# Performance work log

Measured on AMD Instinct MI355X. Metric: run time of the kernel, lower is better.

Reference implementation:

```python
import jax, jax.numpy as jnp
import numpy as np

N = 100000      # total nodes (batched graphs)
E = 1200000     # total edges
A = 256         # annotation size (hidden_size_orig)
H = 64          # gnn_h_size
T = 4           # num_edge_types
STEPS = 6       # num_timesteps
B = 64          # number of graphs in the batch
NUM_CLS = 2


def setup_inputs() -> dict:
    key = jax.random.key(0)
    ks = jax.random.split(key, 16)
    annotation = jax.random.normal(ks[0], (N, A), dtype=jnp.float32)
    src = jax.random.randint(ks[1], (E,), 0, N, dtype=jnp.int32)
    dst = jax.random.randint(ks[2], (E,), 0, N, dtype=jnp.int32)
    etypes = jax.random.randint(ks[3], (E,), 0, T, dtype=jnp.int32)
    graph_ids = jnp.sort(jax.random.randint(ks[4], (N,), 0, B, dtype=jnp.int32))

    def lin(k, fan_in, shape):
        return jax.random.normal(k, shape, dtype=jnp.float32) / np.sqrt(fan_in).astype(np.float32)

    params = {
        'reduce_W': lin(ks[5], A, (A, H)),
        'reduce_b': jnp.zeros((H,), jnp.float32),
        'edge_W': lin(ks[6], H, (T, H, H)),      # per-edge-type linear
        'edge_b': jnp.zeros((T, H), jnp.float32),
        'gru_Wi': lin(ks[7], H, (3 * H, H)),     # torch GRUCell layout: r,z,n
        'gru_bi': jnp.zeros((3 * H,), jnp.float32),
        'gru_Wh': lin(ks[8], H, (3 * H, H)),
        'gru_bh': jnp.zeros((3 * H,), jnp.float32),
        'gate_W': lin(ks[9], 2 * H, (2 * H, 1)),
        'gate_b': jnp.zeros((1,), jnp.float32),
        'out_W': lin(ks[10], 2 * H, (2 * H, NUM_CLS)),
        'out_b': jnp.zeros((NUM_CLS,), jnp.float32),
    }
    return dict(annotation=annotation, src=src, dst=dst, etypes=etypes,
                graph_ids=graph_ids, **params)


def reference(annotation, src, dst, etypes, graph_ids,
              reduce_W, reduce_b, edge_W, edge_b,
              gru_Wi, gru_bi, gru_Wh, gru_bh,
              gate_W, gate_b, out_W, out_b):
    # reduce_layer
    h0 = annotation @ reduce_W + reduce_b            # [N, H]

    def step(h, _):
        # per-edge-type linear on all nodes: [T, N, H]
        transformed = jnp.einsum('nh,thk->tnk', h, edge_W) + edge_b[:, None, :]
        msg = transformed[etypes, src]               # [E, H] gather per edge
        a = jax.ops.segment_sum(msg, dst, num_segments=N)  # scatter-add
        # GRUCell(a, h)
        gi = a @ gru_Wi.T + gru_bi
        gh = h @ gru_Wh.T + gru_bh
        i_r, i_z, i_n = jnp.split(gi, 3, axis=-1)
        h_r, h_z, h_n = jnp.split(gh, 3, axis=-1)
        r = jax.nn.sigmoid(i_r + h_r)
        z = jax.nn.sigmoid(i_z + h_z)
        n = jnp.tanh(i_n + r * h_n)
        h_new = (1.0 - z) * n + z * h
        return h_new, None

    h, _ = jax.lax.scan(step, h0, None, length=STEPS)

    feat = jnp.concatenate([h, h0], axis=-1)         # [N, 2H]

    # GlobalAttentionPooling: segment softmax over gate scores, weighted sum
    gate = feat @ gate_W + gate_b                    # [N, 1]
    gmax = jax.ops.segment_max(gate, graph_ids, num_segments=B)
    gmax = jnp.where(jnp.isfinite(gmax), gmax, 0.0)  # guard empty graphs
    e = jnp.exp(gate - gmax[graph_ids])
    denom = jax.ops.segment_sum(e, graph_ids, num_segments=B)
    alpha = e / denom[graph_ids]                     # [N, 1]
    readout = jax.ops.segment_sum(alpha * feat, graph_ids, num_segments=B)  # [B, 2H]

    logits = readout @ out_W + out_b                 # [B, 2]
    return logits
```

## Files before the change

kernel.cpp:

```cpp
#include <hip/hip_runtime.h>
#include <cstdint>
#include <cstddef>

#define N_NODES 100000
#define N_EDGES 1200000
#define ASIZE 256
#define HSIZE 64
#define NTYPES 4
#define NSTEPS 6
#define NGRAPH 64
#define PS 16

static __device__ __forceinline__ float sigmoidf_(float x) { return 1.0f / (1.0f + expf(-x)); }

__global__ void k_count(const int* __restrict__ dst, int* __restrict__ deg) {
    int e = blockIdx.x * 256 + threadIdx.x;
    if (e < N_EDGES) atomicAdd(&deg[dst[e]], 1);
}

__global__ void k_scan1(const int* __restrict__ deg, int* __restrict__ rs, int* __restrict__ part) {
    __shared__ int sh[256];
    int t = threadIdx.x;
    int base = blockIdx.x * 1024 + t * 4;
    int v0 = (base + 0 < N_NODES) ? deg[base + 0] : 0;
    int v1 = (base + 1 < N_NODES) ? deg[base + 1] : 0;
    int v2 = (base + 2 < N_NODES) ? deg[base + 2] : 0;
    int v3 = (base + 3 < N_NODES) ? deg[base + 3] : 0;
    int s = v0 + v1 + v2 + v3;
    sh[t] = s;
    __syncthreads();
    for (int off = 1; off < 256; off <<= 1) {
        int x = (t >= off) ? sh[t - off] : 0;
        __syncthreads();
        sh[t] += x;
        __syncthreads();
    }
    int excl = sh[t] - s;
    if (t == 255) part[blockIdx.x] = sh[255];
    if (base + 0 < N_NODES) rs[base + 0] = excl;
    if (base + 1 < N_NODES) rs[base + 1] = excl + v0;
    if (base + 2 < N_NODES) rs[base + 2] = excl + v0 + v1;
    if (base + 3 < N_NODES) rs[base + 3] = excl + v0 + v1 + v2;
}

__global__ void k_scan2(int* __restrict__ part, int* __restrict__ rs, int nb) {
    if (threadIdx.x == 0 && blockIdx.x == 0) {
        int run = 0;
        for (int i = 0; i < nb; ++i) { int v = part[i]; part[i] = run; run += v; }
        rs[N_NODES] = run;
    }
}

__global__ void k_scan3(int* __restrict__ rs, const int* __restrict__ part) {
    int i = blockIdx.x * 256 + threadIdx.x;
    if (i < N_NODES) rs[i] += part[i >> 10];
}

__global__ void k_fill(const int* __restrict__ src, const int* __restrict__ dst,
                       const int* __restrict__ ety, const int* __restrict__ rs,
                       int* __restrict__ cur, int* __restrict__ colidx) {
    int e = blockIdx.x * 256 + threadIdx.x;
    if (e < N_EDGES) {
        int d = dst[e];
        int pos = rs[d] + atomicAdd(&cur[d], 1);
        colidx[pos] = src[e] * 256 + ety[e] * 64;
    }
}

__global__ void k_prep2(const float* __restrict__ Wh, const float* __restrict__ Bh,
                        const float* __restrict__ eW, const float* __restrict__ eb,
                        const float* __restrict__ Wi, const float* __restrict__ Bi,
                        float* __restrict__ W256, float* __restrict__ b256,
                        float* __restrict__ Wh192, float* __restrict__ bh192,
                        float* __restrict__ WiA, float* __restrict__ biA) {
    int idx = blockIdx.x * 256 + threadIdx.x;
    if (idx < 64 * 256) {
        int k = idx / 256, c = idx % 256;
        W256[idx] = eW[(size_t)(c >> 6) * 4096 + k * 64 + (c & 63)];
    }
    if (idx < 64 * 192) {
        int k = idx / 192, m = idx % 192;
        int j = m / 3, g = m % 3;
        WiA[idx]   = Wi[(g * 64 + j) * 64 + k];
        Wh192[idx] = Wh[(g * 64 + j) * 64 + k];
    }
    if (idx < 256) b256[idx] = eb[idx];
    if (idx < 192) {
        biA[idx]   = Bi[(idx % 3) * 64 + idx / 3];
        bh192[idx] = Bh[(idx % 3) * 64 + idx / 3];
    }
}

__global__ __launch_bounds__(256) void k_gemm(const float* __restrict__ X, int ldx, int K,
                                              const float* __restrict__ W, int ldw,
                                              const float* __restrict__ bias,
                                              float* __restrict__ Y, float* __restrict__ Y2,
                                              int M) {
    __shared__ float sX[128 * 66];
    __shared__ float sW[64 * 64];
    int tid = threadIdx.x;
    int mtile = blockIdx.x * 64;
    int ntile = blockIdx.y * 128;
    int tc4 = (tid & 15) * 4;
    int tr = tid >> 4;
    float4 acc[8];
#pragma unroll
    for (int i = 0; i < 8; ++i) acc[i] = make_float4(0.f, 0.f, 0.f, 0.f);

    int nkc = K >> 6;
    for (int kc = 0; kc < nkc; ++kc) {
        if (kc) __syncthreads();
#pragma unroll
        for (int i = 0; i < 8; ++i) {
            int lin4 = (i * 256 + tid) * 4;
            int nl = lin4 >> 6, kk = lin4 & 63;
            int n = ntile + nl;
            float4 v = make_float4(0.f, 0.f, 0.f, 0.f);
            if (n < N_NODES) v = *(const float4*)(X + (size_t)n * ldx + kc * 64 + kk);
            float* d = sX + nl * 66 + kk;
            d[0] = v.x; d[1] = v.y; d[2] = v.z; d[3] = v.w;
        }
#pragma unroll
        for (int i = 0; i < 4; ++i) {
            int lin4 = (i * 256 + tid) * 4;
            int kk = lin4 >> 6, c = lin4 & 63;
            float4 v = *(const float4*)(W + (size_t)(kc * 64 + kk) * ldw + mtile + c);
            *(float4*)(sW + kk * 64 + c) = v;
        }
        __syncthreads();
        const float* xr = sX + tr * 8 * 66;
        const float* wr = sW + tc4;
        for (int kk = 0; kk < 64; kk += 2) {
            float4 wA = *(const float4*)(wr + kk * 64);
            float4 wB = *(const float4*)(wr + (kk + 1) * 64);
            float xA[8], xB[8];
#pragma unroll
            for (int i = 0; i < 8; ++i) { xA[i] = xr[i * 66 + kk]; xB[i] = xr[i * 66 + kk + 1]; }
#pragma unroll
            for (int i = 0; i < 8; ++i) {
                acc[i].x = fmaf(xA[i], wA.x, acc[i].x);
                acc[i].y = fmaf(xA[i], wA.y, acc[i].y);
                acc[i].z = fmaf(xA[i], wA.z, acc[i].z);
                acc[i].w = fmaf(xA[i], wA.w, acc[i].w);
            }
#pragma unroll
            for (int i = 0; i < 8; ++i) {
                acc[i].x = fmaf(xB[i], wB.x, acc[i].x);
                acc[i].y = fmaf(xB[i], wB.y, acc[i].y);
                acc[i].z = fmaf(xB[i], wB.z, acc[i].z);
                acc[i].w = fmaf(xB[i], wB.w, acc[i].w);
            }
        }
    }
    float4 bv = *(const float4*)(bias + mtile + tc4);
#pragma unroll
    for (int i = 0; i < 8; ++i) {
        int n = ntile + tr * 8 + i;
        if (n < N_NODES) {
            float4 y;
            y.x = acc[i].x + bv.x; y.y = acc[i].y + bv.y;
            y.z = acc[i].z + bv.z; y.w = acc[i].w + bv.w;
            *(float4*)(Y + (size_t)n * M + mtile + tc4) = y;
            if (Y2) *(float4*)(Y2 + (size_t)n * M + mtile + tc4) = y;
        }
    }
}

__global__ __launch_bounds__(256) void k_gemm_red(const float* __restrict__ X,
                                                  const float* __restrict__ W,
                                                  const float* __restrict__ bias,
                                                  float* __restrict__ Y,
                                                  float* __restrict__ Y2) {
    __shared__ float sX[128 * 66];
    __shared__ float sW[64 * 64];
    int tid = threadIdx.x;
    int ntile = blockIdx.x * 128;
    int tc4 = (tid & 15) * 4;
    int tr = tid >> 4;
    int swr = tid >> 4;
    int swc = (tid & 15) * 4;

    float4 acc[8];
#pragma unroll
    for (int i = 0; i < 8; ++i) acc[i] = make_float4(0.f, 0.f, 0.f, 0.f);

    float4 xreg[8];
    float4 wreg[4];
#pragma unroll
    for (int i = 0; i < 8; ++i) {
        int lin4 = (i * 256 + tid) * 4;
        int nl = lin4 >> 6, kk = lin4 & 63;
        int n = ntile + nl;
        float4 v = make_float4(0.f, 0.f, 0.f, 0.f);
        if (n < N_NODES) v = *(const float4*)(X + (size_t)n * 256 + kk);
        xreg[i] = v;
    }
#pragma unroll
    for (int i = 0; i < 4; ++i)
        wreg[i] = *(const float4*)(W + (size_t)(i * 16 + swr) * 64 + swc);

    for (int kc = 0; kc < 4; ++kc) {
#pragma unroll
        for (int i = 0; i < 8; ++i) {
            int lin4 = (i * 256 + tid) * 4;
            int nl = lin4 >> 6, kk = lin4 & 63;
            float* d = sX + nl * 66 + kk;
            d[0] = xreg[i].x; d[1] = xreg[i].y; d[2] = xreg[i].z; d[3] = xreg[i].w;
        }
#pragma unroll
        for (int i = 0; i < 4; ++i)
            *(float4*)(sW + (i * 16 + swr) * 64 + swc) = wreg[i];
        __syncthreads();
        if (kc < 3) {
#pragma unroll
            for (int i = 0; i < 8; ++i) {
                int lin4 = (i * 256 + tid) * 4;
                int nl = lin4 >> 6, kk = lin4 & 63;
                int n = ntile + nl;
                float4 v = make_float4(0.f, 0.f, 0.f, 0.f);
                if (n < N_NODES) v = *(const float4*)(X + (size_t)n * 256 + (kc + 1) * 64 + kk);
                xreg[i] = v;
            }
#pragma unroll
            for (int i = 0; i < 4; ++i)
                wreg[i] = *(const float4*)(W + (size_t)((kc + 1) * 64 + i * 16 + swr) * 64 + swc);
        }
        const float* xr = sX + tr * 8 * 66;
        const float* wrp = sW + tc4;
        for (int kk = 0; kk < 64; kk += 2) {
            float4 wA = *(const float4*)(wrp + kk * 64);
            float4 wB = *(const float4*)(wrp + (kk + 1) * 64);
            float xA[8], xB[8];
#pragma unroll
            for (int i = 0; i < 8; ++i) { xA[i] = xr[i * 66 + kk]; xB[i] = xr[i * 66 + kk + 1]; }
#pragma unroll
            for (int i = 0; i < 8; ++i) {
                acc[i].x = fmaf(xA[i], wA.x, acc[i].x);
                acc[i].y = fmaf(xA[i], wA.y, acc[i].y);
                acc[i].z = fmaf(xA[i], wA.z, acc[i].z);
                acc[i].w = fmaf(xA[i], wA.w, acc[i].w);
            }
#pragma unroll
            for (int i = 0; i < 8; ++i) {
                acc[i].x = fmaf(xB[i], wB.x, acc[i].x);
                acc[i].y = fmaf(xB[i], wB.y, acc[i].y);
                acc[i].z = fmaf(xB[i], wB.z, acc[i].z);
                acc[i].w = fmaf(xB[i], wB.w, acc[i].w);
            }
        }
        if (kc < 3) __syncthreads();
    }
    float4 bv = *(const float4*)(bias + tc4);
#pragma unroll
    for (int i = 0; i < 8; ++i) {
        int n = ntile + tr * 8 + i;
        if (n < N_NODES) {
            float4 y;
            y.x = acc[i].x + bv.x; y.y = acc[i].y + bv.y;
            y.z = acc[i].z + bv.z; y.w = acc[i].w + bv.w;
            *(float4*)(Y + (size_t)n * 64 + tc4) = y;
            *(float4*)(Y2 + (size_t)n * 64 + tc4) = y;
        }
    }
}

__global__ void k_aggregate(const float* __restrict__ buf1, const int* __restrict__ rs,
                            const int* __restrict__ colidx, float* __restrict__ a) {
    int l = threadIdx.x & 63;
    int n = blockIdx.x * 4 + (threadIdx.x >> 6);
    int sub = l >> 4;
    int kq = (l & 15) * 4;
    int beg = rs[n], end = rs[n + 1];
    float4 acc = make_float4(0.f, 0.f, 0.f, 0.f);
    int s = beg;
    for (; s + 31 < end; s += 32) {
        int c0 = colidx[s + sub];
        int c1 = colidx[s + 4 + sub];
        int c2 = colidx[s + 8 + sub];
        int c3 = colidx[s + 12 + sub];
        int c4 = colidx[s + 16 + sub];
        int c5 = colidx[s + 20 + sub];
        int c6 = colidx[s + 24 + sub];
        int c7 = colidx[s + 28 + sub];
        float4 v0 = *(const float4*)(buf1 + (size_t)c0 + kq);
        float4 v1 = *(const float4*)(buf1 + (size_t)c1 + kq);
        float4 v2 = *(const float4*)(buf1 + (size_t)c2 + kq);
        float4 v3 = *(const float4*)(buf1 + (size_t)c3 + kq);
        float4 v4 = *(const float4*)(buf1 + (size_t)c4 + kq);
        float4 v5 = *(const float4*)(buf1 + (size_t)c5 + kq);
        float4 v6 = *(const float4*)(buf1 + (size_t)c6 + kq);
        float4 v7 = *(const float4*)(buf1 + (size_t)c7 + kq);
        acc.x += v0.x; acc.y += v0.y; acc.z += v0.z; acc.w += v0.w;
        acc.x += v1.x; acc.y += v1.y; acc.z += v1.z; acc.w += v1.w;
        acc.x += v2.x; acc.y += v2.y; acc.z += v2.z; acc.w += v2.w;
        acc.x += v3.x; acc.y += v3.y; acc.z += v3.z; acc.w += v3.w;
        acc.x += v4.x; acc.y += v4.y; acc.z += v4.z; acc.w += v4.w;
        acc.x += v5.x; acc.y += v5.y; acc.z += v5.z; acc.w += v5.w;
        acc.x += v6.x; acc.y += v6.y; acc.z += v6.z; acc.w += v6.w;
        acc.x += v7.x; acc.y += v7.y; acc.z += v7.z; acc.w += v7.w;
    }
    for (; s + 3 < end; s += 4) {
        int c = colidx[s + sub];
        float4 v = *(const float4*)(buf1 + (size_t)c + kq);
        acc.x += v.x; acc.y += v.y; acc.z += v.z; acc.w += v.w;
    }
    for (; s < end; ++s) {
        if (sub == 0) {
            int c = colidx[s];
            float4 v = *(const float4*)(buf1 + (size_t)c + kq);
            acc.x += v.x; acc.y += v.y; acc.z += v.z; acc.w += v.w;
        }
    }
    float4 t;
    t.x = acc.x + __shfl_xor(acc.x, 16, 64);
    t.y = acc.y + __shfl_xor(acc.y, 16, 64);
    t.z = acc.z + __shfl_xor(acc.z, 16, 64);
    t.w = acc.w + __shfl_xor(acc.w, 16, 64);
    float4 r;
    r.x = t.x + __shfl_xor(t.x, 32, 64);
    r.y = t.y + __shfl_xor(t.y, 32, 64);
    r.z = t.z + __shfl_xor(t.z, 32, 64);
    r.w = t.w + __shfl_xor(t.w, 32, 64);
    if (sub == 0) *(float4*)(a + (size_t)n * 64 + kq) = r;
}

__global__ __launch_bounds__(256) void k_gruF3(const float* __restrict__ A,
                                               const float* __restrict__ WiA,
                                               const float* __restrict__ biA,
                                               const float* __restrict__ Wh192,
                                               const float* __restrict__ bh192,
                                               const float* __restrict__ W256,
                                               const float* __restrict__ b256,
                                               float* __restrict__ H,
                                               float* __restrict__ buf1,
                                               int do_trans) {
    __shared__ float sXT[32 * 68];
    __shared__ float sW[32 * 192];
    __shared__ float sHT[64 * 68];
    int tid = threadIdx.x;
    int ntile = blockIdx.x * 64;
    int tc = tid & 15;
    int tr = tid >> 4;
    float acc[2][4][12];
#pragma unroll
    for (int p = 0; p < 2; ++p)
#pragma unroll
        for (int i = 0; i < 4; ++i)
#pragma unroll
            for (int c = 0; c < 12; ++c) acc[p][i][c] = 0.f;

#pragma unroll
    for (int ph = 0; ph < 2; ++ph) {
        const float* Xsrc = (ph == 0) ? A : H;
        const float* Wsrc = (ph == 0) ? WiA : Wh192;
        for (int kc = 0; kc < 2; ++kc) {
            if (ph || kc) __syncthreads();
#pragma unroll
            for (int i = 0; i < 2; ++i) {
                int lin = i * 256 + tid;
                int nl = lin >> 3;
                int kk = (lin & 7) * 4;
                int n = ntile + nl;
                float4 v = make_float4(0.f, 0.f, 0.f, 0.f);
                if (n < N_NODES) v = *(const float4*)(Xsrc + (size_t)n * 64 + kc * 32 + kk);
                sXT[(kk + 0) * 68 + nl] = v.x;
                sXT[(kk + 1) * 68 + nl] = v.y;
                sXT[(kk + 2) * 68 + nl] = v.z;
                sXT[(kk + 3) * 68 + nl] = v.w;
            }
            {
                int kk = tid >> 3, c = (tid & 7) * 24;
                const float* srcp = Wsrc + (size_t)(kc * 32 + kk) * 192 + c;
                float* d = sW + kk * 192 + c;
#pragma unroll
                for (int u = 0; u < 6; ++u) *(float4*)(d + 4 * u) = *(const float4*)(srcp + 4 * u);
            }
            __syncthreads();
            const float* wr = sW + tc * 12;
            for (int kk = 0; kk < 32; kk += 2) {
                float4 w0 = *(const float4*)(wr + kk * 192);
                float4 w1 = *(const float4*)(wr + kk * 192 + 4);
                float4 w2 = *(const float4*)(wr + kk * 192 + 8);
                float4 u0 = *(const float4*)(wr + (kk + 1) * 192);
                float4 u1 = *(const float4*)(wr + (kk + 1) * 192 + 4);
                float4 u2 = *(const float4*)(wr + (kk + 1) * 192 + 8);
                float4 xA4 = *(const float4*)(sXT + kk * 68 + tr * 4);
                float4 xB4 = *(const float4*)(sXT + (kk + 1) * 68 + tr * 4);
                float xA[4] = {xA4.x, xA4.y, xA4.z, xA4.w};
                float xB[4] = {xB4.x, xB4.y, xB4.z, xB4.w};
#pragma unroll
                for (int i = 0; i < 4; ++i) {
                    acc[ph][i][0]  = fmaf(xA[i], w0.x, acc[ph][i][0]);
                    acc[ph][i][1]  = fmaf(xA[i], w0.y, acc[ph][i][1]);
                    acc[ph][i][2]  = fmaf(xA[i], w0.z, acc[ph][i][2]);
                    acc[ph][i][3]  = fmaf(xA[i], w0.w, acc[ph][i][3]);
                    acc[ph][i][4]  = fmaf(xA[i], w1.x, acc[ph][i][4]);
                    acc[ph][i][5]  = fmaf(xA[i], w1.y, acc[ph][i][5]);
                    acc[ph][i][6]  = fmaf(xA[i], w1.z, acc[ph][i][6]);
                    acc[ph][i][7]  = fmaf(xA[i], w1.w, acc[ph][i][7]);
                    acc[ph][i][8]  = fmaf(xA[i], w2.x, acc[ph][i][8]);
                    acc[ph][i][9]  = fmaf(xA[i], w2.y, acc[ph][i][9]);
                    acc[ph][i][10] = fmaf(xA[i], w2.z, acc[ph][i][10]);
                    acc[ph][i][11] = fmaf(xA[i], w2.w, acc[ph][i][11]);
                }
#pragma unroll
                for (int i = 0; i < 4; ++i) {
                    acc[ph][i][0]  = fmaf(xB[i], u0.x, acc[ph][i][0]);
                    acc[ph][i][1]  = fmaf(xB[i], u0.y, acc[ph][i][1]);
                    acc[ph][i][2]  = fmaf(xB[i], u0.z, acc[ph][i][2]);
                    acc[ph][i][3]  = fmaf(xB[i], u0.w, acc[ph][i][3]);
                    acc[ph][i][4]  = fmaf(xB[i], u1.x, acc[ph][i][4]);
                    acc[ph][i][5]  = fmaf(xB[i], u1.y, acc[ph][i][5]);
                    acc[ph][i][6]  = fmaf(xB[i], u1.z, acc[ph][i][6]);
                    acc[ph][i][7]  = fmaf(xB[i], u1.w, acc[ph][i][7]);
                    acc[ph][i][8]  = fmaf(xB[i], u2.x, acc[ph][i][8]);
                    acc[ph][i][9]  = fmaf(xB[i], u2.y, acc[ph][i][9]);
                    acc[ph][i][10] = fmaf(xB[i], u2.z, acc[ph][i][10]);
                    acc[ph][i][11] = fmaf(xB[i], u2.w, acc[ph][i][11]);
                }
            }
        }
    }
    float bb[12], bh[12];
    {
        float4 b0 = *(const float4*)(biA + tc * 12);
        float4 b1 = *(const float4*)(biA + tc * 12 + 4);
        float4 b2 = *(const float4*)(biA + tc * 12 + 8);
        bb[0] = b0.x; bb[1] = b0.y; bb[2] = b0.z; bb[3] = b0.w;
        bb[4] = b1.x; bb[5] = b1.y; bb[6] = b1.z; bb[7] = b1.w;
        bb[8] = b2.x; bb[9] = b2.y; bb[10] = b2.z; bb[11] = b2.w;
        float4 c0 = *(const float4*)(bh192 + tc * 12);
        float4 c1 = *(const float4*)(bh192 + tc * 12 + 4);
        float4 c2 = *(const float4*)(bh192 + tc * 12 + 8);
        bh[0] = c0.x; bh[1] = c0.y; bh[2] = c0.z; bh[3] = c0.w;
        bh[4] = c1.x; bh[5] = c1.y; bh[6] = c1.z; bh[7] = c1.w;
        bh[8] = c2.x; bh[9] = c2.y; bh[10] = c2.z; bh[11] = c2.w;
    }
#pragma unroll
    for (int i = 0; i < 4; ++i) {
        int n = ntile + tr * 4 + i;
        if (n >= N_NODES) continue;
        float gg[12];
#pragma unroll
        for (int c = 0; c < 12; ++c) gg[c] = acc[1][i][c] + bh[c];
        float4 hv = *(const float4*)(H + (size_t)n * 64 + tc * 4);
        float res[4];
#pragma unroll
        for (int jj = 0; jj < 4; ++jj) {
            int c = jj * 3;
            float r = sigmoidf_(acc[0][i][c] + bb[c] + gg[c]);
            float z = sigmoidf_(acc[0][i][c + 1] + bb[c + 1] + gg[c + 1]);
            float nn = tanhf(acc[0][i][c + 2] + bb[c + 2] + r * gg[c + 2]);
            float hj = (jj == 0) ? hv.x : (jj == 1) ? hv.y : (jj == 2) ? hv.z : hv.w;
            res[jj] = (1.f - z) * nn + z * hj;
        }
        float4 o; o.x = res[0]; o.y = res[1]; o.z = res[2]; o.w = res[3];
        *(float4*)(H + (size_t)n * 64 + tc * 4) = o;
        if (do_trans) {
#pragma unroll
            for (int jj = 0; jj < 4; ++jj)
                sHT[(tc * 4 + jj) * 68 + (tr * 4 + i)] = res[jj];
        }
    }
    if (do_trans) {
        __syncthreads();
        int tc2 = tc * 4;
        for (int mt = 0; mt < 4; ++mt) {
            if (mt) __syncthreads();
#pragma unroll
            for (int i = 0; i < 4; ++i) {
                int idx = i * 256 + tid;
                int row = idx >> 4, c4 = (idx & 15) * 4;
                *(float4*)(sW + row * 64 + c4) =
                    *(const float4*)(W256 + (size_t)row * 256 + mt * 64 + c4);
            }
            __syncthreads();
            float4 tacc[4];
#pragma unroll
            for (int i = 0; i < 4; ++i) tacc[i] = make_float4(0.f, 0.f, 0.f, 0.f);
            for (int kk = 0; kk < 64; kk += 2) {
                float4 wA = *(const float4*)(sW + kk * 64 + tc2);
                float4 wB = *(const float4*)(sW + (kk + 1) * 64 + tc2);
                float4 xA4 = *(const float4*)(sHT + kk * 68 + tr * 4);
                float4 xB4 = *(const float4*)(sHT + (kk + 1) * 68 + tr * 4);
                float xA[4] = {xA4.x, xA4.y, xA4.z, xA4.w};
                float xB[4] = {xB4.x, xB4.y, xB4.z, xB4.w};
#pragma unroll
                for (int i = 0; i < 4; ++i) {
                    tacc[i].x = fmaf(xA[i], wA.x, tacc[i].x);
                    tacc[i].y = fmaf(xA[i], wA.y, tacc[i].y);
                    tacc[i].z = fmaf(xA[i], wA.z, tacc[i].z);
                    tacc[i].w = fmaf(xA[i], wA.w, tacc[i].w);
                }
#pragma unroll
                for (int i = 0; i < 4; ++i) {
                    tacc[i].x = fmaf(xB[i], wB.x, tacc[i].x);
                    tacc[i].y = fmaf(xB[i], wB.y, tacc[i].y);
                    tacc[i].z = fmaf(xB[i], wB.z, tacc[i].z);
                    tacc[i].w = fmaf(xB[i], wB.w, tacc[i].w);
                }
            }
            float4 bv = *(const float4*)(b256 + mt * 64 + tc2);
#pragma unroll
            for (int i = 0; i < 4; ++i) {
                int n = ntile + tr * 4 + i;
                if (n < N_NODES) {
                    float4 y;
                    y.x = tacc[i].x + bv.x; y.y = tacc[i].y + bv.y;
                    y.z = tacc[i].z + bv.z; y.w = tacc[i].w + bv.w;
                    *(float4*)(buf1 + (size_t)n * 256 + mt * 64 + tc2) = y;
                }
            }
        }
    }
}

__global__ void k_bounds(const int* __restrict__ gid, int* __restrict__ start) {
    int n = blockIdx.x * 256 + threadIdx.x;
    if (n < N_NODES) {
        int g = gid[n];
        if (n == 0) {
            for (int x = 0; x <= g; ++x) start[x] = 0;
        } else {
            int pg = gid[n - 1];
            for (int x = pg + 1; x <= g; ++x) start[x] = n;
        }
        if (n == N_NODES - 1) {
            for (int x = g + 1; x <= NGRAPH; ++x) start[x] = N_NODES;
        }
    }
}

__global__ void k_gate2(const float* __restrict__ H, const float* __restrict__ H0,
                        const float* __restrict__ gW, const float* __restrict__ gb,
                        float* __restrict__ gate) {
    int l = threadIdx.x & 63;
    int n = blockIdx.x * 4 + (threadIdx.x >> 6);
    float v = H[(size_t)n * 64 + l] * gW[l] + H0[(size_t)n * 64 + l] * gW[64 + l];
    for (int off = 32; off > 0; off >>= 1) v += __shfl_xor(v, off, 64);
    if (l == 0) gate[n] = v + gb[0];
}

__global__ __launch_bounds__(64) void k_poolA(const float* __restrict__ gate,
                                              const int* __restrict__ start,
                                              float* __restrict__ pmax) {
    int g = blockIdx.x, s = blockIdx.y;
    int beg = start[g], len = start[g + 1] - beg;
    int sb = beg + (int)((long long)len * s / PS);
    int se = beg + (int)((long long)len * (s + 1) / PS);
    float m = -INFINITY;
    for (int n = sb + threadIdx.x; n < se; n += 64) m = fmaxf(m, gate[n]);
    for (int off = 32; off > 0; off >>= 1) m = fmaxf(m, __shfl_xor(m, off, 64));
    if (threadIdx.x == 0) pmax[g * PS + s] = m;
}

__global__ void k_poolB(const float* __restrict__ pmax, float* __restrict__ gm) {
    int g = threadIdx.x;
    float m = -INFINITY;
    for (int s = 0; s < PS; ++s) m = fmaxf(m, pmax[g * PS + s]);
    if (!isfinite(m)) m = 0.0f;
    gm[g] = m;
}

__global__ __launch_bounds__(256) void k_poolC(const float* __restrict__ H,
                                               const float* __restrict__ H0,
                                               const float* __restrict__ gate,
                                               const int* __restrict__ start,
                                               const float* __restrict__ gm,
                                               float* __restrict__ pnum,
                                               float* __restrict__ pden) {
    int g = blockIdx.x, s = blockIdx.y;
    int beg = start[g], len = start[g + 1] - beg;
    int sb = beg + (int)((long long)len * s / PS);
    int se = beg + (int)((long long)len * (s + 1) / PS);
    int t = threadIdx.x;
    int lane = t & 63, wave = t >> 6;
    float m = gm[g];
    __shared__ float shh[4][64], sh0[4][64], ses[4];
    float ah = 0.f, ah0 = 0.f, es = 0.f;
    for (int n = sb + wave; n < se; n += 4) {
        float e = expf(gate[n] - m);
        es += e;
        ah  += e * H [(size_t)n * 64 + lane];
        ah0 += e * H0[(size_t)n * 64 + lane];
    }
    shh[wave][lane] = ah; sh0[wave][lane] = ah0;
    if (lane == 0) ses[wave] = es;
    __syncthreads();
    if (wave == 0) {
        float r  = shh[0][lane] + shh[1][lane] + shh[2][lane] + shh[3][lane];
        float r0 = sh0[0][lane] + sh0[1][lane] + sh0[2][lane] + sh0[3][lane];
        int base = (g * PS + s) * 128;
        pnum[base + lane]      = r;
        pnum[base + 64 + lane] = r0;
        if (lane == 0) pden[g * PS + s] = ses[0] + ses[1] + ses[2] + ses[3];
    }
}

__global__ __launch_bounds__(128) void k_poolD(const float* __restrict__ pnum,
                                               const float* __restrict__ pden,
                                               float* __restrict__ ro) {
    int g = blockIdx.x;
    int c = threadIdx.x;
    float den = 0.f;
    for (int s = 0; s < PS; ++s) den += pden[g * PS + s];
    float nu = 0.f;
    for (int s = 0; s < PS; ++s) nu += pnum[(g * PS + s) * 128 + c];
    ro[g * 128 + c] = (den > 0.f) ? nu / den : 0.f;
}

__global__ void k_logits(const float* __restrict__ ro, const float* __restrict__ oW,
                         const float* __restrict__ ob, float* __restrict__ out) {
    int t = threadIdx.x;
    int b = t >> 1;
    int c = t & 1;
    float acc = ob[c];
    for (int k = 0; k < 128; ++k) acc = fmaf(ro[b * 128 + k], oW[k * 2 + c], acc);
    out[b * 2 + c] = acc;
}

extern "C" void kernel_launch(void* const* d_in, const int* in_sizes, int n_in,
                              void* d_out, int out_size, void* d_ws, size_t ws_size,
                              hipStream_t stream) {
    (void)in_sizes; (void)n_in; (void)out_size; (void)ws_size;
    const float* ann = (const float*)d_in[0];
    const int* src   = (const int*)d_in[1];
    const int* dst   = (const int*)d_in[2];
    const int* ety   = (const int*)d_in[3];
    const int* gid   = (const int*)d_in[4];
    const float* rW  = (const float*)d_in[5];
    const float* rb  = (const float*)d_in[6];
    const float* eW  = (const float*)d_in[7];
    const float* eb  = (const float*)d_in[8];
    const float* Wi  = (const float*)d_in[9];
    const float* Bi  = (const float*)d_in[10];
    const float* Wh  = (const float*)d_in[11];
    const float* Bh  = (const float*)d_in[12];
    const float* gW  = (const float*)d_in[13];
    const float* gb  = (const float*)d_in[14];
    const float* oW  = (const float*)d_in[15];
    const float* ob  = (const float*)d_in[16];
    float* out = (float*)d_out;

    char* p = (char*)d_ws;
    auto take = [&](size_t nbytes) -> void* {
        void* r = (void*)p;
        p += (nbytes + 255) & ~((size_t)255);
        return r;
    };
    float* h0      = (float*)take((size_t)N_NODES * 64 * 4);
    float* h       = (float*)take((size_t)N_NODES * 64 * 4);
    float* abuf    = (float*)take((size_t)N_NODES * 64 * 4);
    float* buf1    = (float*)take((size_t)N_NODES * 256 * 4);
    float* W256    = (float*)take(64 * 256 * 4);
    float* b256    = (float*)take(256 * 4);
    float* Wh192   = (float*)take(64 * 192 * 4);
    float* bh192   = (float*)take(192 * 4);
    float* WiA     = (float*)take(64 * 192 * 4);
    float* biA     = (float*)take(192 * 4);
    int* deg       = (int*)take((size_t)N_NODES * 4);
    int* cur       = (int*)take((size_t)N_NODES * 4);
    int* rs        = (int*)take((size_t)(N_NODES + 1) * 4);
    int* part      = (int*)take(512);
    int* colidx    = (int*)take((size_t)N_EDGES * 4);
    float* gate    = (float*)take((size_t)N_NODES * 4);
    int* start     = (int*)take((size_t)(NGRAPH + 1) * 4);
    float* pmax    = (float*)take(NGRAPH * PS * 4);
    float* gm      = (float*)take(NGRAPH * 4);
    float* pnum    = (float*)take((size_t)NGRAPH * PS * 128 * 4);
    float* pden    = (float*)take(NGRAPH * PS * 4);
    float* ro      = (float*)take(NGRAPH * 128 * 4);

    hipMemsetAsync(deg, 0, (size_t)N_NODES * 4, stream);
    hipMemsetAsync(cur, 0, (size_t)N_NODES * 4, stream);
    k_count<<<(N_EDGES + 255) / 256, 256, 0, stream>>>(dst, deg);
    int nb = (N_NODES + 1023) / 1024;
    k_scan1<<<nb, 256, 0, stream>>>(deg, rs, part);
    k_scan2<<<1, 64, 0, stream>>>(part, rs, nb);
    k_scan3<<<(N_NODES + 255) / 256, 256, 0, stream>>>(rs, part);
    k_fill<<<(N_EDGES + 255) / 256, 256, 0, stream>>>(src, dst, ety, rs, cur, colidx);

    k_prep2<<<112, 256, 0, stream>>>(Wh, Bh, eW, eb, Wi, Bi, W256, b256, Wh192, bh192, WiA, biA);
    k_bounds<<<(N_NODES + 255) / 256, 256, 0, stream>>>(gid, start);

    int ntiles = (N_NODES + 127) / 128;

    k_gemm_red<<<ntiles, 256, 0, stream>>>(ann, rW, rb, h, h0);

    k_gemm<<<dim3(4, ntiles), 256, 0, stream>>>(h, 64, 64, W256, 256, b256,
                                                buf1, nullptr, 256);

    for (int s = 0; s < NSTEPS; ++s) {
        k_aggregate<<<N_NODES / 4, 256, 0, stream>>>(buf1, rs, colidx, abuf);
        k_gruF3<<<(N_NODES + 63) / 64, 256, 0, stream>>>(abuf, WiA, biA, Wh192, bh192,
                                                         W256, b256, h, buf1,
                                                         (s < NSTEPS - 1) ? 1 : 0);
    }

    k_gate2<<<N_NODES / 4, 256, 0, stream>>>(h, h0, gW, gb, gate);
    k_poolA<<<dim3(NGRAPH, PS), 64, 0, stream>>>(gate, start, pmax);
    k_poolB<<<1, 64, 0, stream>>>(pmax, gm);
    k_poolC<<<dim3(NGRAPH, PS), 256, 0, stream>>>(h, h0, gate, start, gm, pnum, pden);
    k_poolD<<<NGRAPH, 128, 0, stream>>>(pnum, pden, ro);
    k_logits<<<1, 128, 0, stream>>>(ro, oW, ob, out);
}
```

Before: 1.513 ms.

## Read GRU weights directly from global memory and batch aggregate tail gathers

The GRU kernel no longer stages the weight tiles in shared memory. Each thread instead loads its weight float4s straight from global memory, relying on the L1/L2 cache, which removes the shared-memory weight buffer and several block barriers and may raise occupancy. The aggregate kernel's remaining groups of four edges are now loaded in one unrolled batch of up to seven gathers before accumulating, which increases memory-level parallelism in the tail. In exchange, every thread reissues global weight loads that shared memory previously served, so performance depends on cache hit rates.

Measured after the change: 1.787 ms. 1.18x slower.

```diff
diff --git a/kernel.cpp b/kernel.cpp
--- a/kernel.cpp
+++ b/kernel.cpp
@@ -271,9 +271,11 @@
     int sub = l >> 4;
     int kq = (l & 15) * 4;
     int beg = rs[n], end = rs[n + 1];
+    int deg = end - beg;
+    int c4end = beg + (deg & ~3);
     float4 acc = make_float4(0.f, 0.f, 0.f, 0.f);
     int s = beg;
-    for (; s + 31 < end; s += 32) {
+    for (; s + 31 < c4end; s += 32) {
         int c0 = colidx[s + sub];
         int c1 = colidx[s + 4 + sub];
         int c2 = colidx[s + 8 + sub];
@@ -299,10 +301,23 @@
         acc.x += v6.x; acc.y += v6.y; acc.z += v6.z; acc.w += v6.w;
         acc.x += v7.x; acc.y += v7.y; acc.z += v7.z; acc.w += v7.w;
     }
-    for (; s + 3 < end; s += 4) {
-        int c = colidx[s + sub];
-        float4 v = *(const float4*)(buf1 + (size_t)c + kq);
-        acc.x += v.x; acc.y += v.y; acc.z += v.z; acc.w += v.w;
+    {
+        int nv = (c4end - s) >> 2;
+        float4 vv[7];
+#pragma unroll
+        for (int k = 0; k < 7; ++k) {
+            if (k < nv) {
+                int c = colidx[s + k * 4 + sub];
+                vv[k] = *(const float4*)(buf1 + (size_t)c + kq);
+            }
+        }
+#pragma unroll
+        for (int k = 0; k < 7; ++k) {
+            if (k < nv) {
+                acc.x += vv[k].x; acc.y += vv[k].y; acc.z += vv[k].z; acc.w += vv[k].w;
+            }
+        }
+        s += nv * 4;
     }
     for (; s < end; ++s) {
         if (sub == 0) {
@@ -335,7 +350,6 @@
                                                float* __restrict__ buf1,
                                                int do_trans) {
     __shared__ float sXT[32 * 68];
-    __shared__ float sW[32 * 192];
     __shared__ float sHT[64 * 68];
     int tid = threadIdx.x;
     int ntile = blockIdx.x * 64;
@@ -368,22 +382,15 @@
                 sXT[(kk + 2) * 68 + nl] = v.z;
                 sXT[(kk + 3) * 68 + nl] = v.w;
             }
-            {
-                int kk = tid >> 3, c = (tid & 7) * 24;
-                const float* srcp = Wsrc + (size_t)(kc * 32 + kk) * 192 + c;
-                float* d = sW + kk * 192 + c;
-#pragma unroll
-                for (int u = 0; u < 6; ++u) *(float4*)(d + 4 * u) = *(const float4*)(srcp + 4 * u);
-            }
             __syncthreads();
-            const float* wr = sW + tc * 12;
+            const float* wg = Wsrc + (size_t)(kc * 32) * 192 + tc * 12;
             for (int kk = 0; kk < 32; kk += 2) {
-                float4 w0 = *(const float4*)(wr + kk * 192);
-                float4 w1 = *(const float4*)(wr + kk * 192 + 4);
-                float4 w2 = *(const float4*)(wr + kk * 192 + 8);
-                float4 u0 = *(const float4*)(wr + (kk + 1) * 192);
-                float4 u1 = *(const float4*)(wr + (kk + 1) * 192 + 4);
-                float4 u2 = *(const float4*)(wr + (kk + 1) * 192 + 8);
+                float4 w0 = *(const float4*)(wg + kk * 192);
+                float4 w1 = *(const float4*)(wg + kk * 192 + 4);
+                float4 w2 = *(const float4*)(wg + kk * 192 + 8);
+                float4 u0 = *(const float4*)(wg + (kk + 1) * 192);
+                float4 u1 = *(const float4*)(wg + (kk + 1) * 192 + 4);
+                float4 u2 = *(const float4*)(wg + (kk + 1) * 192 + 8);
                 float4 xA4 = *(const float4*)(sXT + kk * 68 + tr * 4);
                 float4 xB4 = *(const float4*)(sXT + (kk + 1) * 68 + tr * 4);
                 float xA[4] = {xA4.x, xA4.y, xA4.z, xA4.w};
@@ -466,21 +473,13 @@
         __syncthreads();
         int tc2 = tc * 4;
         for (int mt = 0; mt < 4; ++mt) {
-            if (mt) __syncthreads();
-#pragma unroll
-            for (int i = 0; i < 4; ++i) {
-                int idx = i * 256 + tid;
-                int row = idx >> 4, c4 = (idx & 15) * 4;
-                *(float4*)(sW + row * 64 + c4) =
-                    *(const float4*)(W256 + (size_t)row * 256 + mt * 64 + c4);
-            }
-            __syncthreads();
+            const float* wg2 = W256 + mt * 64 + tc2;
             float4 tacc[4];
 #pragma unroll
             for (int i = 0; i < 4; ++i) tacc[i] = make_float4(0.f, 0.f, 0.f, 0.f);
             for (int kk = 0; kk < 64; kk += 2) {
-                float4 wA = *(const float4*)(sW + kk * 64 + tc2);
-                float4 wB = *(const float4*)(sW + (kk + 1) * 64 + tc2);
+                float4 wA = *(const float4*)(wg2 + (size_t)kk * 256);
+                float4 wB = *(const float4*)(wg2 + (size_t)(kk + 1) * 256);
                 float4 xA4 = *(const float4*)(sHT + kk * 68 + tr * 4);
                 float4 xB4 = *(const float4*)(sHT + (kk + 1) * 68 + tr * 4);
                 float xA[4] = {xA4.x, xA4.y, xA4.z, xA4.w};
```

## Fuse neighbor aggregation into GRU kernel with ping-pong message buffers

Applied to the files above, without the earlier changes.

The separate aggregate kernel is folded into the GRU kernel: each block first gathers and sums neighbor messages for its 64 nodes straight into a transposed shared tile, then runs the GRU GEMMs from shared memory. This removes the global round trip of the aggregated buffer and one launch per step. Because blocks now read messages while other blocks write the next step's messages, two buffers alternate per step. The cost is lower gather parallelism per block (4 waves do 64 nodes serially, with fewer blocks in flight), which may hurt latency hiding for the irregular gather.

New measurement: 1.811 ms. 1.2x slower.

```diff
diff --git a/kernel.cpp b/kernel.cpp
--- a/kernel.cpp
+++ b/kernel.cpp
@@ -264,67 +264,9 @@
     }
 }
 
-__global__ void k_aggregate(const float* __restrict__ buf1, const int* __restrict__ rs,
-                            const int* __restrict__ colidx, float* __restrict__ a) {
-    int l = threadIdx.x & 63;
-    int n = blockIdx.x * 4 + (threadIdx.x >> 6);
-    int sub = l >> 4;
-    int kq = (l & 15) * 4;
-    int beg = rs[n], end = rs[n + 1];
-    float4 acc = make_float4(0.f, 0.f, 0.f, 0.f);
-    int s = beg;
-    for (; s + 31 < end; s += 32) {
-        int c0 = colidx[s + sub];
-        int c1 = colidx[s + 4 + sub];
-        int c2 = colidx[s + 8 + sub];
-        int c3 = colidx[s + 12 + sub];
-        int c4 = colidx[s + 16 + sub];
-        int c5 = colidx[s + 20 + sub];
-        int c6 = colidx[s + 24 + sub];
-        int c7 = colidx[s + 28 + sub];
-        float4 v0 = *(const float4*)(buf1 + (size_t)c0 + kq);
-        float4 v1 = *(const float4*)(buf1 + (size_t)c1 + kq);
-        float4 v2 = *(const float4*)(buf1 + (size_t)c2 + kq);
-        float4 v3 = *(const float4*)(buf1 + (size_t)c3 + kq);
-        float4 v4 = *(const float4*)(buf1 + (size_t)c4 + kq);
-        float4 v5 = *(const float4*)(buf1 + (size_t)c5 + kq);
-        float4 v6 = *(const float4*)(buf1 + (size_t)c6 + kq);
-        float4 v7 = *(const float4*)(buf1 + (size_t)c7 + kq);
-        acc.x += v0.x; acc.y += v0.y; acc.z += v0.z; acc.w += v0.w;
-        acc.x += v1.x; acc.y += v1.y; acc.z += v1.z; acc.w += v1.w;
-        acc.x += v2.x; acc.y += v2.y; acc.z += v2.z; acc.w += v2.w;
-        acc.x += v3.x; acc.y += v3.y; acc.z += v3.z; acc.w += v3.w;
-        acc.x += v4.x; acc.y += v4.y; acc.z += v4.z; acc.w += v4.w;
-        acc.x += v5.x; acc.y += v5.y; acc.z += v5.z; acc.w += v5.w;
-        acc.x += v6.x; acc.y += v6.y; acc.z += v6.z; acc.w += v6.w;
-        acc.x += v7.x; acc.y += v7.y; acc.z += v7.z; acc.w += v7.w;
-    }
-    for (; s + 3 < end; s += 4) {
-        int c = colidx[s + sub];
-        float4 v = *(const float4*)(buf1 + (size_t)c + kq);
-        acc.x += v.x; acc.y += v.y; acc.z += v.z; acc.w += v.w;
-    }
-    for (; s < end; ++s) {
-        if (sub == 0) {
-            int c = colidx[s];
-            float4 v = *(const float4*)(buf1 + (size_t)c + kq);
-            acc.x += v.x; acc.y += v.y; acc.z += v.z; acc.w += v.w;
-        }
-    }
-    float4 t;
-    t.x = acc.x + __shfl_xor(acc.x, 16, 64);
-    t.y = acc.y + __shfl_xor(acc.y, 16, 64);
-    t.z = acc.z + __shfl_xor(acc.z, 16, 64);
-    t.w = acc.w + __shfl_xor(acc.w, 16, 64);
-    float4 r;
-    r.x = t.x + __shfl_xor(t.x, 32, 64);
-    r.y = t.y + __shfl_xor(t.y, 32, 64);
-    r.z = t.z + __shfl_xor(t.z, 32, 64);
-    r.w = t.w + __shfl_xor(t.w, 32, 64);
-    if (sub == 0) *(float4*)(a + (size_t)n * 64 + kq) = r;
-}
-
-__global__ __launch_bounds__(256) void k_gruF3(const float* __restrict__ A,
+__global__ __launch_bounds__(256) void k_gruF5(const float* __restrict__ bufIn,
+                                               const int* __restrict__ rs,
+                                               const int* __restrict__ colidx,
                                                const float* __restrict__ WiA,
                                                const float* __restrict__ biA,
                                                const float* __restrict__ Wh192,
@@ -332,13 +274,97 @@
                                                const float* __restrict__ W256,
                                                const float* __restrict__ b256,
                                                float* __restrict__ H,
-                                               float* __restrict__ buf1,
+                                               float* __restrict__ bufOut,
                                                int do_trans) {
+    __shared__ float sAT[64 * 68];
+    __shared__ float sW[32 * 192];
     __shared__ float sXT[32 * 68];
-    __shared__ float sW[32 * 192];
-    __shared__ float sHT[64 * 68];
     int tid = threadIdx.x;
     int ntile = blockIdx.x * 64;
+    int lane = tid & 63;
+    int wv = tid >> 6;
+    int sub = lane >> 4;
+    int kq = (lane & 15) * 4;
+
+    for (int j = 0; j < 16; ++j) {
+        int nl = wv * 16 + j;
+        int n = ntile + nl;
+        if (n < N_NODES) {
+            int beg = rs[n], end = rs[n + 1];
+            int dg = end - beg;
+            int c4end = beg + (dg & ~3);
+            float4 a4 = make_float4(0.f, 0.f, 0.f, 0.f);
+            int s = beg;
+            for (; s + 31 < c4end; s += 32) {
+                int c0 = colidx[s + sub];
+                int c1 = colidx[s + 4 + sub];
+                int c2 = colidx[s + 8 + sub];
+                int c3 = colidx[s + 12 + sub];
+                int c4 = colidx[s + 16 + sub];
+                int c5 = colidx[s + 20 + sub];
+                int c6 = colidx[s + 24 + sub];
+                int c7 = colidx[s + 28 + sub];
+                float4 v0 = *(const float4*)(bufIn + (size_t)c0 + kq);
+                float4 v1 = *(const float4*)(bufIn + (size_t)c1 + kq);
+                float4 v2 = *(const float4*)(bufIn + (size_t)c2 + kq);
+                float4 v3 = *(const float4*)(bufIn + (size_t)c3 + kq);
+                float4 v4 = *(const float4*)(bufIn + (size_t)c4 + kq);
+                float4 v5 = *(const float4*)(bufIn + (size_t)c5 + kq);
+                float4 v6 = *(const float4*)(bufIn + (size_t)c6 + kq);
+                float4 v7 = *(const float4*)(bufIn + (size_t)c7 + kq);
+                a4.x += v0.x; a4.y += v0.y; a4.z += v0.z; a4.w += v0.w;
+                a4.x += v1.x; a4.y += v1.y; a4.z += v1.z; a4.w += v1.w;
+                a4.x += v2.x; a4.y += v2.y; a4.z += v2.z; a4.w += v2.w;
+                a4.x += v3.x; a4.y += v3.y; a4.z += v3.z; a4.w += v3.w;
+                a4.x += v4.x; a4.y += v4.y; a4.z += v4.z; a4.w += v4.w;
+                a4.x += v5.x; a4.y += v5.y; a4.z += v5.z; a4.w += v5.w;
+                a4.x += v6.x; a4.y += v6.y; a4.z += v6.z; a4.w += v6.w;
+                a4.x += v7.x; a4.y += v7.y; a4.z += v7.z; a4.w += v7.w;
+            }
+            {
+                int nv = (c4end - s) >> 2;
+                float4 vv[7];
+#pragma unroll
+                for (int k = 0; k < 7; ++k) {
+                    if (k < nv) {
+                        int c = colidx[s + k * 4 + sub];
+                        vv[k] = *(const float4*)(bufIn + (size_t)c + kq);
+                    }
+                }
+#pragma unroll
+                for (int k = 0; k < 7; ++k) {
+                    if (k < nv) {
+                        a4.x += vv[k].x; a4.y += vv[k].y; a4.z += vv[k].z; a4.w += vv[k].w;
+                    }
+                }
+                s += nv * 4;
+            }
+            for (; s < end; ++s) {
+                if (sub == 0) {
+                    int c = colidx[s];
+                    float4 v = *(const float4*)(bufIn + (size_t)c + kq);
+                    a4.x += v.x; a4.y += v.y; a4.z += v.z; a4.w += v.w;
+                }
+            }
+            float4 t4;
+            t4.x = a4.x + __shfl_xor(a4.x, 16, 64);
+            t4.y = a4.y + __shfl_xor(a4.y, 16, 64);
+            t4.z = a4.z + __shfl_xor(a4.z, 16, 64);
+            t4.w = a4.w + __shfl_xor(a4.w, 16, 64);
+            float4 r4;
+            r4.x = t4.x + __shfl_xor(t4.x, 32, 64);
+            r4.y = t4.y + __shfl_xor(t4.y, 32, 64);
+            r4.z = t4.z + __shfl_xor(t4.z, 32, 64);
+            r4.w = t4.w + __shfl_xor(t4.w, 32, 64);
+            if (sub == 0) {
+                sAT[(kq + 0) * 68 + nl] = r4.x;
+                sAT[(kq + 1) * 68 + nl] = r4.y;
+                sAT[(kq + 2) * 68 + nl] = r4.z;
+                sAT[(kq + 3) * 68 + nl] = r4.w;
+            }
+        }
+    }
+
     int tc = tid & 15;
     int tr = tid >> 4;
     float acc[2][4][12];
@@ -349,78 +375,86 @@
 #pragma unroll
             for (int c = 0; c < 12; ++c) acc[p][i][c] = 0.f;
 
-#pragma unroll
-    for (int ph = 0; ph < 2; ++ph) {
-        const float* Xsrc = (ph == 0) ? A : H;
-        const float* Wsrc = (ph == 0) ? WiA : Wh192;
-        for (int kc = 0; kc < 2; ++kc) {
-            if (ph || kc) __syncthreads();
-#pragma unroll
-            for (int i = 0; i < 2; ++i) {
-                int lin = i * 256 + tid;
-                int nl = lin >> 3;
-                int kk = (lin & 7) * 4;
-                int n = ntile + nl;
-                float4 v = make_float4(0.f, 0.f, 0.f, 0.f);
-                if (n < N_NODES) v = *(const float4*)(Xsrc + (size_t)n * 64 + kc * 32 + kk);
-                sXT[(kk + 0) * 68 + nl] = v.x;
-                sXT[(kk + 1) * 68 + nl] = v.y;
-                sXT[(kk + 2) * 68 + nl] = v.z;
-                sXT[(kk + 3) * 68 + nl] = v.w;
-            }
-            {
-                int kk = tid >> 3, c = (tid & 7) * 24;
-                const float* srcp = Wsrc + (size_t)(kc * 32 + kk) * 192 + c;
-                float* d = sW + kk * 192 + c;
-#pragma unroll
-                for (int u = 0; u < 6; ++u) *(float4*)(d + 4 * u) = *(const float4*)(srcp + 4 * u);
-            }
-            __syncthreads();
-            const float* wr = sW + tc * 12;
-            for (int kk = 0; kk < 32; kk += 2) {
-                float4 w0 = *(const float4*)(wr + kk * 192);
-                float4 w1 = *(const float4*)(wr + kk * 192 + 4);
-                float4 w2 = *(const float4*)(wr + kk * 192 + 8);
-                float4 u0 = *(const float4*)(wr + (kk + 1) * 192);
-                float4 u1 = *(const float4*)(wr + (kk + 1) * 192 + 4);
-                float4 u2 = *(const float4*)(wr + (kk + 1) * 192 + 8);
-                float4 xA4 = *(const float4*)(sXT + kk * 68 + tr * 4);
-                float4 xB4 = *(const float4*)(sXT + (kk + 1) * 68 + tr * 4);
-                float xA[4] = {xA4.x, xA4.y, xA4.z, xA4.w};
-                float xB[4] = {xB4.x, xB4.y, xB4.z, xB4.w};
-#pragma unroll
-                for (int i = 0; i < 4; ++i) {
-                    acc[ph][i][0]  = fmaf(xA[i], w0.x, acc[ph][i][0]);
-                    acc[ph][i][1]  = fmaf(xA[i], w0.y, acc[ph][i][1]);
-                    acc[ph][i][2]  = fmaf(xA[i], w0.z, acc[ph][i][2]);
-                    acc[ph][i][3]  = fmaf(xA[i], w0.w, acc[ph][i][3]);
-                    acc[ph][i][4]  = fmaf(xA[i], w1.x, acc[ph][i][4]);
-                    acc[ph][i][5]  = fmaf(xA[i], w1.y, acc[ph][i][5]);
-                    acc[ph][i][6]  = fmaf(xA[i], w1.z, acc[ph][i][6]);
-                    acc[ph][i][7]  = fmaf(xA[i], w1.w, acc[ph][i][7]);
-                    acc[ph][i][8]  = fmaf(xA[i], w2.x, acc[ph][i][8]);
-                    acc[ph][i][9]  = fmaf(xA[i], w2.y, acc[ph][i][9]);
-                    acc[ph][i][10] = fmaf(xA[i], w2.z, acc[ph][i][10]);
-                    acc[ph][i][11] = fmaf(xA[i], w2.w, acc[ph][i][11]);
-                }
-#pragma unroll
-                for (int i = 0; i < 4; ++i) {
-                    acc[ph][i][0]  = fmaf(xB[i], u0.x, acc[ph][i][0]);
-                    acc[ph][i][1]  = fmaf(xB[i], u0.y, acc[ph][i][1]);
-                    acc[ph][i][2]  = fmaf(xB[i], u0.z, acc[ph][i][2]);
-                    acc[ph][i][3]  = fmaf(xB[i], u0.w, acc[ph][i][3]);
-                    acc[ph][i][4]  = fmaf(xB[i], u1.x, acc[ph][i][4]);
-                    acc[ph][i][5]  = fmaf(xB[i], u1.y, acc[ph][i][5]);
-                    acc[ph][i][6]  = fmaf(xB[i], u1.z, acc[ph][i][6]);
-                    acc[ph][i][7]  = fmaf(xB[i], u1.w, acc[ph][i][7]);
-                    acc[ph][i][8]  = fmaf(xB[i], u2.x, acc[ph][i][8]);
-                    acc[ph][i][9]  = fmaf(xB[i], u2.y, acc[ph][i][9]);
-                    acc[ph][i][10] = fmaf(xB[i], u2.z, acc[ph][i][10]);
-                    acc[ph][i][11] = fmaf(xB[i], u2.w, acc[ph][i][11]);
-                }
-            }
-        }
-    }
+    int nl0 = tid >> 3;
+    int nl1 = (256 + tid) >> 3;
+    int kks = (tid & 7) * 4;
+    int nn0 = ntile + nl0, nn1 = ntile + nl1;
+    int kkr = tid >> 3, wcc = (tid & 7) * 24;
+
+    for (int c = 0; c < 4; ++c) {
+        int isgh = (c < 2);
+        int kc = c & 1;
+        int ph = isgh ? 1 : 0;
+        const float* Wsrc = isgh ? Wh192 : WiA;
+        if (c) __syncthreads();
+        if (isgh) {
+            float4 v0 = make_float4(0.f, 0.f, 0.f, 0.f);
+            float4 v1 = make_float4(0.f, 0.f, 0.f, 0.f);
+            if (nn0 < N_NODES) v0 = *(const float4*)(H + (size_t)nn0 * 64 + kc * 32 + kks);
+            if (nn1 < N_NODES) v1 = *(const float4*)(H + (size_t)nn1 * 64 + kc * 32 + kks);
+            sXT[(kks + 0) * 68 + nl0] = v0.x;
+            sXT[(kks + 1) * 68 + nl0] = v0.y;
+            sXT[(kks + 2) * 68 + nl0] = v0.z;
+            sXT[(kks + 3) * 68 + nl0] = v0.w;
+            sXT[(kks + 0) * 68 + nl1] = v1.x;
+            sXT[(kks + 1) * 68 + nl1] = v1.y;
+            sXT[(kks + 2) * 68 + nl1] = v1.z;
+            sXT[(kks + 3) * 68 + nl1] = v1.w;
+        }
+        {
+            const float* srcp = Wsrc + (size_t)(kc * 32 + kkr) * 192 + wcc;
+            float* d = sW + kkr * 192 + wcc;
+#pragma unroll
+            for (int u = 0; u < 6; ++u) *(float4*)(d + 4 * u) = *(const float4*)(srcp + 4 * u);
+        }
+        __syncthreads();
+        const float* wr = sW + tc * 12;
+        const float* xbase = isgh ? sXT : (sAT + (size_t)(kc * 32) * 68);
+        for (int kk = 0; kk < 32; kk += 2) {
+            float4 w0 = *(const float4*)(wr + kk * 192);
+            float4 w1 = *(const float4*)(wr + kk * 192 + 4);
+            float4 w2 = *(const float4*)(wr + kk * 192 + 8);
+            float4 u0 = *(const float4*)(wr + (kk + 1) * 192);
+            float4 u1 = *(const float4*)(wr + (kk + 1) * 192 + 4);
+            float4 u2 = *(const float4*)(wr + (kk + 1) * 192 + 8);
+            float4 xA4 = *(const float4*)(xbase + kk * 68 + tr * 4);
+            float4 xB4 = *(const float4*)(xbase + (kk + 1) * 68 + tr * 4);
+            float xA[4] = {xA4.x, xA4.y, xA4.z, xA4.w};
+            float xB[4] = {xB4.x, xB4.y, xB4.z, xB4.w};
+#pragma unroll
+            for (int i = 0; i < 4; ++i) {
+                acc[ph][i][0]  = fmaf(xA[i], w0.x, acc[ph][i][0]);
+                acc[ph][i][1]  = fmaf(xA[i], w0.y, acc[ph][i][1]);
+                acc[ph][i][2]  = fmaf(xA[i], w0.z, acc[ph][i][2]);
+                acc[ph][i][3]  = fmaf(xA[i], w0.w, acc[ph][i][3]);
+                acc[ph][i][4]  = fmaf(xA[i], w1.x, acc[ph][i][4]);
+                acc[ph][i][5]  = fmaf(xA[i], w1.y, acc[ph][i][5]);
+                acc[ph][i][6]  = fmaf(xA[i], w1.z, acc[ph][i][6]);
+                acc[ph][i][7]  = fmaf(xA[i], w1.w, acc[ph][i][7]);
+                acc[ph][i][8]  = fmaf(xA[i], w2.x, acc[ph][i][8]);
+                acc[ph][i][9]  = fmaf(xA[i], w2.y, acc[ph][i][9]);
+                acc[ph][i][10] = fmaf(xA[i], w2.z, acc[ph][i][10]);
+                acc[ph][i][11] = fmaf(xA[i], w2.w, acc[ph][i][11]);
+            }
+#pragma unroll
+            for (int i = 0; i < 4; ++i) {
+                acc[ph][i][0]  = fmaf(xB[i], u0.x, acc[ph][i][0]);
+                acc[ph][i][1]  = fmaf(xB[i], u0.y, acc[ph][i][1]);
+                acc[ph][i][2]  = fmaf(xB[i], u0.z, acc[ph][i][2]);
+                acc[ph][i][3]  = fmaf(xB[i], u0.w, acc[ph][i][3]);
+                acc[ph][i][4]  = fmaf(xB[i], u1.x, acc[ph][i][4]);
+                acc[ph][i][5]  = fmaf(xB[i], u1.y, acc[ph][i][5]);
+                acc[ph][i][6]  = fmaf(xB[i], u1.z, acc[ph][i][6]);
+                acc[ph][i][7]  = fmaf(xB[i], u1.w, acc[ph][i][7]);
+                acc[ph][i][8]  = fmaf(xB[i], u2.x, acc[ph][i][8]);
+                acc[ph][i][9]  = fmaf(xB[i], u2.y, acc[ph][i][9]);
+                acc[ph][i][10] = fmaf(xB[i], u2.z, acc[ph][i][10]);
+                acc[ph][i][11] = fmaf(xB[i], u2.w, acc[ph][i][11]);
+            }
+        }
+    }
+    __syncthreads();
+
     float bb[12], bh[12];
     {
         float4 b0 = *(const float4*)(biA + tc * 12);
@@ -459,7 +493,7 @@
         if (do_trans) {
 #pragma unroll
             for (int jj = 0; jj < 4; ++jj)
-                sHT[(tc * 4 + jj) * 68 + (tr * 4 + i)] = res[jj];
+                sAT[(tc * 4 + jj) * 68 + (tr * 4 + i)] = res[jj];
         }
     }
     if (do_trans) {
@@ -481,8 +515,8 @@
             for (int kk = 0; kk < 64; kk += 2) {
                 float4 wA = *(const float4*)(sW + kk * 64 + tc2);
                 float4 wB = *(const float4*)(sW + (kk + 1) * 64 + tc2);
-                float4 xA4 = *(const float4*)(sHT + kk * 68 + tr * 4);
-                float4 xB4 = *(const float4*)(sHT + (kk + 1) * 68 + tr * 4);
+                float4 xA4 = *(const float4*)(sAT + kk * 68 + tr * 4);
+                float4 xB4 = *(const float4*)(sAT + (kk + 1) * 68 + tr * 4);
                 float xA[4] = {xA4.x, xA4.y, xA4.z, xA4.w};
                 float xB[4] = {xB4.x, xB4.y, xB4.z, xB4.w};
 #pragma unroll
@@ -508,7 +542,7 @@
                     float4 y;
                     y.x = tacc[i].x + bv.x; y.y = tacc[i].y + bv.y;
                     y.z = tacc[i].z + bv.z; y.w = tacc[i].w + bv.w;
-                    *(float4*)(buf1 + (size_t)n * 256 + mt * 64 + tc2) = y;
+                    *(float4*)(bufOut + (size_t)n * 256 + mt * 64 + tc2) = y;
                 }
             }
         }
@@ -650,8 +684,8 @@
     };
     float* h0      = (float*)take((size_t)N_NODES * 64 * 4);
     float* h       = (float*)take((size_t)N_NODES * 64 * 4);
-    float* abuf    = (float*)take((size_t)N_NODES * 64 * 4);
     float* buf1    = (float*)take((size_t)N_NODES * 256 * 4);
+    float* buf2    = (float*)take((size_t)N_NODES * 256 * 4);
     float* W256    = (float*)take(64 * 256 * 4);
     float* b256    = (float*)take(256 * 4);
     float* Wh192   = (float*)take(64 * 192 * 4);
@@ -690,11 +724,13 @@
     k_gemm<<<dim3(4, ntiles), 256, 0, stream>>>(h, 64, 64, W256, 256, b256,
                                                 buf1, nullptr, 256);
 
+    int nblk = (N_NODES + 63) / 64;
     for (int s = 0; s < NSTEPS; ++s) {
-        k_aggregate<<<N_NODES / 4, 256, 0, stream>>>(buf1, rs, colidx, abuf);
-        k_gruF3<<<(N_NODES + 63) / 64, 256, 0, stream>>>(abuf, WiA, biA, Wh192, bh192,
-                                                         W256, b256, h, buf1,
-                                                         (s < NSTEPS - 1) ? 1 : 0);
+        float* bin  = (s & 1) ? buf2 : buf1;
+        float* bout = (s & 1) ? buf1 : buf2;
+        k_gruF5<<<nblk, 256, 0, stream>>>(bin, rs, colidx, WiA, biA, Wh192, bh192,
+                                          W256, b256, h, bout,
+                                          (s < NSTEPS - 1) ? 1 : 0);
     }
 
     k_gate2<<<N_NODES / 4, 256, 0, stream>>>(h, h0, gW, gb, gate);
```
